# Kernel optimization log

Measured on AMD Instinct MI355X. Metric: run time of the kernel, lower is better.

The kernel has to match this reference:

```python
import jax, jax.numpy as jnp
import numpy as np

R = 1.1
SCALE = 100.0
BUMP_STEPS = 32
NUM_THETAS = 32
NUM_FEATURES = 128
N_NODES = 200000
NUM_GRAPHS = 128


def setup_inputs() -> dict:
    key = jax.random.key(0)
    k1, k2, k3 = jax.random.split(key, 3)
    x = jax.random.normal(k1, (N_NODES, NUM_FEATURES), dtype=jnp.float32)
    batch = jnp.sort(jax.random.randint(k2, (N_NODES,), 0, NUM_GRAPHS, dtype=jnp.int64))
    v = jax.random.uniform(k3, (NUM_THETAS, NUM_FEATURES), dtype=jnp.float32) - 0.5
    return {"x": x, "batch": batch, "num_graphs": NUM_GRAPHS, "v": v}


def reference(x, batch, num_graphs, v):
    # nh: node heights along each direction theta -> [N, T]
    nh = x @ v.T
    # linspace over filtration values -> [S]
    lin = jnp.linspace(-R, R, BUMP_STEPS, dtype=nh.dtype)
    # bump: sigmoid difference; second point is the constant pad value R
    # ecc: [N, S, T]  (node-major so segment_sum reduces the leading axis)
    ecc = (jax.nn.sigmoid(SCALE * (lin[None, :, None] - nh[:, None, :]))
           - jax.nn.sigmoid(SCALE * (lin - R))[None, :, None])
    # scatter-add per graph label -> [ng, S, T] == index_add over dim1 then movedim(0,1)
    ect = jax.ops.segment_sum(ecc, batch, num_segments=num_graphs)
    return ect
```

## Files before the change

kernel.cpp:

```cpp
#include <hip/hip_runtime.h>
#include <math.h>

#define NF 128
#define NT 32
#define NS 32
#define ATILE 64
#define ABLOCKS 3125
#define VSTRIDE 136
#define HPAD 33

typedef short bf16x8 __attribute__((ext_vector_type(8)));
typedef float floatx4 __attribute__((ext_vector_type(4)));

__device__ __forceinline__ float rcp_fast(float x) { return __builtin_amdgcn_rcpf(x); }

__device__ __forceinline__ void split_bf16(float f, unsigned short& h, unsigned short& l) {
    unsigned u  = __float_as_uint(f);
    unsigned r  = u + 0x7FFFu + ((u >> 16) & 1u);
    unsigned hb = r & 0xFFFF0000u;
    h = (unsigned short)(hb >> 16);
    float rem = f - __uint_as_float(hb);
    unsigned u2 = __float_as_uint(rem);
    unsigned r2 = u2 + 0x7FFFu + ((u2 >> 16) & 1u);
    l = (unsigned short)(r2 >> 16);
}

__device__ __forceinline__ void split8(float4 a, float4 b, bf16x8& h8, bf16x8& l8) {
    unsigned short h[8], l[8];
    split_bf16(a.x, h[0], l[0]); split_bf16(a.y, h[1], l[1]);
    split_bf16(a.z, h[2], l[2]); split_bf16(a.w, h[3], l[3]);
    split_bf16(b.x, h[4], l[4]); split_bf16(b.y, h[5], l[5]);
    split_bf16(b.z, h[6], l[6]); split_bf16(b.w, h[7], l[7]);
    h8 = (bf16x8){(short)h[0],(short)h[1],(short)h[2],(short)h[3],
                  (short)h[4],(short)h[5],(short)h[6],(short)h[7]};
    l8 = (bf16x8){(short)l[0],(short)l[1],(short)l[2],(short)l[3],
                  (short)l[4],(short)l[5],(short)l[6],(short)l[7]};
}

__global__ __launch_bounds__(256, 7)
void ect_fused(const float* __restrict__ x,
               const int* __restrict__ batch,
               const float* __restrict__ v,
               float* __restrict__ out)
{
    __shared__ __align__(16) unsigned short vh[NT * VSTRIDE];
    __shared__ __align__(16) unsigned short vl[NT * VSTRIDE];
    __shared__ int   batch_lds[ATILE];
    __shared__ float corr[NT * HPAD];
    __shared__ float cnt_lds;
    __shared__ int   qcnt[4];

    const int tid  = threadIdx.x;
    const int blk  = blockIdx.x;
    const int w    = tid >> 6;
    const int lane = tid & 63;
    const int mrow = lane & 15;
    const int quad = lane >> 4;

    #pragma unroll
    for (int j = 0; j < 4; ++j) {
        int idx4 = j * 256 + tid;
        int row  = idx4 >> 5;
        int f4   = idx4 & 31;
        float4 val = *(const float4*)&v[(size_t)row * NF + f4 * 4];
        unsigned short h0,h1,h2,h3,l0,l1,l2,l3;
        split_bf16(val.x, h0, l0); split_bf16(val.y, h1, l1);
        split_bf16(val.z, h2, l2); split_bf16(val.w, h3, l3);
        uint2 hh, ll;
        hh.x = (unsigned)h0 | ((unsigned)h1 << 16); hh.y = (unsigned)h2 | ((unsigned)h3 << 16);
        ll.x = (unsigned)l0 | ((unsigned)l1 << 16); ll.y = (unsigned)l2 | ((unsigned)l3 << 16);
        *(uint2*)&vh[row * VSTRIDE + f4 * 4] = hh;
        *(uint2*)&vl[row * VSTRIDE + f4 * 4] = ll;
    }
    if (tid < ATILE) batch_lds[tid] = batch[blk * ATILE + tid];

    const size_t arow = (size_t)blk * ATILE + w * 16 + mrow;
    const float* __restrict__ xrow = x + arow * NF + quad * 8;

    floatx4 acc0 = {0.f, 0.f, 0.f, 0.f};
    floatx4 acc1 = {0.f, 0.f, 0.f, 0.f};

    bf16x8 ah[4], al[4];
    #pragma unroll
    for (int slice = 0; slice < 4; ++slice) {
        float4 a0 = *(const float4*)&xrow[slice * 32];
        float4 a1 = *(const float4*)&xrow[slice * 32 + 4];
        split8(a0, a1, ah[slice], al[slice]);
    }
    __syncthreads();

    const int b0base = mrow * VSTRIDE + quad * 8;
    const int b1base = (16 + mrow) * VSTRIDE + quad * 8;
    #pragma unroll
    for (int slice = 0; slice < 4; ++slice) {
        bf16x8 bh0 = *(bf16x8*)&vh[b0base + slice * 32];
        bf16x8 bl0 = *(bf16x8*)&vl[b0base + slice * 32];
        bf16x8 bh1 = *(bf16x8*)&vh[b1base + slice * 32];
        bf16x8 bl1 = *(bf16x8*)&vl[b1base + slice * 32];
        acc0 = __builtin_amdgcn_mfma_f32_16x16x32_bf16(ah[slice], bh0, acc0, 0, 0, 0);
        acc0 = __builtin_amdgcn_mfma_f32_16x16x32_bf16(ah[slice], bl0, acc0, 0, 0, 0);
        acc0 = __builtin_amdgcn_mfma_f32_16x16x32_bf16(al[slice], bh0, acc0, 0, 0, 0);
        acc1 = __builtin_amdgcn_mfma_f32_16x16x32_bf16(ah[slice], bh1, acc1, 0, 0, 0);
        acc1 = __builtin_amdgcn_mfma_f32_16x16x32_bf16(ah[slice], bl1, acc1, 0, 0, 0);
        acc1 = __builtin_amdgcn_mfma_f32_16x16x32_bf16(al[slice], bh1, acc1, 0, 0, 0);
    }
    __syncthreads();

    float* qf = (float*)vh;

    const float inv_dlin = 14.090909090909092f;
    const float Lw       = 10.23848093f;
    const float dlin     = 2.2f / 31.0f;
    const float L        = 144.26950408889634f;
    const float C1       = 8.2777115e-04f;

    const int g_first = batch_lds[0];
    const int g_last  = batch_lds[ATILE - 1];

    const int ft = tid & 31;
    const int sb = tid >> 5;
    float csk[4];
    #pragma unroll
    for (int k = 0; k < 4; ++k) {
        int s = sb + 8 * k;
        float lin_s = -1.1f + (float)s * dlin;
        csk[k] = rcp_fast(1.0f + __builtin_amdgcn_exp2f(L * (1.1f - lin_s)));
    }

    const float cH0 = 31.5f + 64.0f * (float)mrow;
    const float cH1 = cH0 + 1024.0f;
    const float lo0 = cH0 - 16.95f, hi0 = cH0 + 16.95f;
    const float lo1 = cH1 - 16.95f, hi1 = cH1 + 16.95f;

    for (int gp = g_first; gp <= g_last; ++gp) {
        for (int i = tid; i < NT * HPAD; i += 256) corr[i] = 0.0f;
        if (tid < ATILE) {
            unsigned long long m2 = __ballot(batch_lds[tid] == gp);
            if (tid == 0) cnt_lds = (float)__popcll(m2);
        }
        int wbase = w * 512;
        int c0 = 0, c1 = 0;
        #pragma unroll
        for (int reg = 0; reg < 4; ++reg) {
            bool ok = (batch_lds[w * 16 + quad * 4 + reg] == gp);
            {
                float zt = fmaf(acc0[reg], inv_dlin, cH0);
                bool full = ok && (zt > lo0) && (zt < hi0);
                unsigned long long m = __ballot(full);
                int pos = __builtin_amdgcn_mbcnt_hi((unsigned)(m >> 32),
                          __builtin_amdgcn_mbcnt_lo((unsigned)m, 0));
                if (full) qf[wbase + pos] = zt;
                wbase += __popcll(m);
                c0 += (ok && (zt <= lo0)) ? 1 : 0;
            }
            {
                float zt = fmaf(acc1[reg], inv_dlin, cH1);
                bool full = ok && (zt > lo1) && (zt < hi1);
                unsigned long long m = __ballot(full);
                int pos = __builtin_amdgcn_mbcnt_hi((unsigned)(m >> 32),
                          __builtin_amdgcn_mbcnt_lo((unsigned)m, 0));
                if (full) qf[wbase + pos] = zt;
                wbase += __popcll(m);
                c1 += (ok && (zt <= lo1)) ? 1 : 0;
            }
        }
        if (lane == 0) qcnt[w] = wbase - w * 512;
        __syncthreads();

        if (c0) atomicAdd(&corr[mrow * HPAD], (float)c0);
        if (c1) atomicAdd(&corr[(16 + mrow) * HPAD], (float)c1);
        for (int seg = 0; seg < 4; ++seg) {
            const int ne = qcnt[seg];
            for (int i = tid; i < ne; i += 256) {
                float zt  = qf[seg * 512 + i];
                float tf  = floorf(zt * 0.015625f);
                float z   = fmaf(tf, -64.0f, zt) - 16.0f;
                int   b   = (int)tf * HPAD;
                float s0f = ceilf(z - 1.45f);
                int   s0  = (int)s0f;
                float e0  = __builtin_amdgcn_exp2f(Lw * (z - s0f));
                float e1  = e0 * C1;
                float e2  = e1 * C1;
                float f0  = rcp_fast(1.0f + e0);
                float f1  = rcp_fast(1.0f + e1);
                float f2  = rcp_fast(1.0f + e2);
                int sA = max(s0, 0);
                atomicAdd(&corr[b + sA], f0);
                int sB = max(s0 + 1, 0);
                if (sB < 32) atomicAdd(&corr[b + sB], f1 - f0);
                int sC = max(s0 + 2, 0);
                if (sC < 32) atomicAdd(&corr[b + sC], f2 - f1);
                int sD = s0 + 3;
                if (sD < 32) atomicAdd(&corr[b + sD], 1.0f - f2);
            }
        }
        __syncthreads();

        {
            const int grp = tid >> 5;
            const int sc  = tid & 31;
            for (int row = grp; row < NT; row += 8) {
                float val = corr[row * HPAD + sc];
                #pragma unroll
                for (int d = 1; d < 32; d <<= 1) {
                    float nbr = __shfl_up(val, d, 32);
                    if (sc >= d) val += nbr;
                }
                corr[row * HPAD + sc] = val;
            }
        }
        __syncthreads();

        #pragma unroll
        for (int k = 0; k < 4; ++k) {
            int s = sb + 8 * k;
            float val = corr[ft * HPAD + s] - cnt_lds * csk[k];
            atomicAdd(&out[(size_t)gp * (NS * NT) + s * NT + ft], val);
        }
        if (gp < g_last) __syncthreads();
    }
}

extern "C" void kernel_launch(void* const* d_in, const int* in_sizes, int n_in,
                              void* d_out, int out_size, void* d_ws, size_t ws_size,
                              hipStream_t stream) {
    const float* x     = (const float*)d_in[0];
    const int*   batch = (const int*)d_in[1];
    const float* v     = (const float*)d_in[3];
    float*       out   = (float*)d_out;

    hipMemsetAsync(d_out, 0, (size_t)out_size * sizeof(float), stream);
    ect_fused<<<dim3(ABLOCKS), dim3(256), 0, stream>>>(x, batch, v, out);
}
```

Before: 183.6 us.

## Double node tile per block and deposit bumps directly instead of compacting

Each block now handles 128 nodes in two MFMA passes, which halves the block count and the per-block fixed costs: splitting v into bf16 hi/lo, the per-graph corr reset and scan, and the global atomics to out. The ballot-based compaction queue in LDS and the separate loop that drained it are removed. Each lane now computes the sigmoid terms for its own in-window heights and adds them into corr with LDS atomics. The divergent per-lane deposits may leave SIMD lanes idle, and the occupancy hint drops from 7 to 5 blocks per CU, which lowers latency hiding.

```diff
diff --git a/kernel.cpp b/kernel.cpp
--- a/kernel.cpp
+++ b/kernel.cpp
@@ -1,11 +1,12 @@
 #include <hip/hip_runtime.h>
 #include <math.h>
 
+#define N_NODES 200000
 #define NF 128
 #define NT 32
 #define NS 32
-#define ATILE 64
-#define ABLOCKS 3125
+#define ATILE 128
+#define ABLOCKS 1563
 #define VSTRIDE 136
 #define HPAD 33
 
@@ -37,7 +38,22 @@
                   (short)l[4],(short)l[5],(short)l[6],(short)l[7]};
 }
 
-__global__ __launch_bounds__(256, 7)
+__device__ __forceinline__ void deposit(float* corr, int b, float z, float Lw, float C1) {
+    float s0f = ceilf(z - 1.45f);
+    int   s0  = (int)s0f;
+    float e0  = __builtin_amdgcn_exp2f(Lw * (z - s0f));
+    float e1  = e0 * C1;
+    float e2  = e1 * C1;
+    float f0  = rcp_fast(1.0f + e0);
+    float f1  = rcp_fast(1.0f + e1);
+    float f2  = rcp_fast(1.0f + e2);
+    atomicAdd(&corr[b + max(s0, 0)], f0);
+    int sB = max(s0 + 1, 0); if (sB < 32) atomicAdd(&corr[b + sB], f1 - f0);
+    int sC = max(s0 + 2, 0); if (sC < 32) atomicAdd(&corr[b + sC], f2 - f1);
+    int sD = s0 + 3;         if (sD < 32) atomicAdd(&corr[b + sD], 1.0f - f2);
+}
+
+__global__ __launch_bounds__(256, 5)
 void ect_fused(const float* __restrict__ x,
                const int* __restrict__ batch,
                const float* __restrict__ v,
@@ -47,8 +63,7 @@
     __shared__ __align__(16) unsigned short vl[NT * VSTRIDE];
     __shared__ int   batch_lds[ATILE];
     __shared__ float corr[NT * HPAD];
-    __shared__ float cnt_lds;
-    __shared__ int   qcnt[4];
+    __shared__ float cnt_part[2];
 
     const int tid  = threadIdx.x;
     const int blk  = blockIdx.x;
@@ -72,19 +87,27 @@
         *(uint2*)&vh[row * VSTRIDE + f4 * 4] = hh;
         *(uint2*)&vl[row * VSTRIDE + f4 * 4] = ll;
     }
-    if (tid < ATILE) batch_lds[tid] = batch[blk * ATILE + tid];
-
-    const size_t arow = (size_t)blk * ATILE + w * 16 + mrow;
-    const float* __restrict__ xrow = x + arow * NF + quad * 8;
-
-    floatx4 acc0 = {0.f, 0.f, 0.f, 0.f};
-    floatx4 acc1 = {0.f, 0.f, 0.f, 0.f};
+    const int base   = blk * ATILE;
+    const int nvalid = min(ATILE, N_NODES - base);
+    if (tid < ATILE) {
+        int gi = base + tid;
+        batch_lds[tid] = (gi < N_NODES) ? batch[gi] : -1;
+    }
+
+    const int r0  = w * 16 + mrow;
+    const int gi0 = min(base + r0,      N_NODES - 1);
+    const int gi1 = min(base + 64 + r0, N_NODES - 1);
+    const float* __restrict__ x0 = x + (size_t)gi0 * NF + quad * 8;
+    const float* __restrict__ x1 = x + (size_t)gi1 * NF + quad * 8;
+
+    floatx4 acc0[2] = {(floatx4){0.f,0.f,0.f,0.f}, (floatx4){0.f,0.f,0.f,0.f}};
+    floatx4 acc1[2] = {(floatx4){0.f,0.f,0.f,0.f}, (floatx4){0.f,0.f,0.f,0.f}};
 
     bf16x8 ah[4], al[4];
     #pragma unroll
     for (int slice = 0; slice < 4; ++slice) {
-        float4 a0 = *(const float4*)&xrow[slice * 32];
-        float4 a1 = *(const float4*)&xrow[slice * 32 + 4];
+        float4 a0 = *(const float4*)&x0[slice * 32];
+        float4 a1 = *(const float4*)&x0[slice * 32 + 4];
         split8(a0, a1, ah[slice], al[slice]);
     }
     __syncthreads();
@@ -97,16 +120,32 @@
         bf16x8 bl0 = *(bf16x8*)&vl[b0base + slice * 32];
         bf16x8 bh1 = *(bf16x8*)&vh[b1base + slice * 32];
         bf16x8 bl1 = *(bf16x8*)&vl[b1base + slice * 32];
-        acc0 = __builtin_amdgcn_mfma_f32_16x16x32_bf16(ah[slice], bh0, acc0, 0, 0, 0);
-        acc0 = __builtin_amdgcn_mfma_f32_16x16x32_bf16(ah[slice], bl0, acc0, 0, 0, 0);
-        acc0 = __builtin_amdgcn_mfma_f32_16x16x32_bf16(al[slice], bh0, acc0, 0, 0, 0);
-        acc1 = __builtin_amdgcn_mfma_f32_16x16x32_bf16(ah[slice], bh1, acc1, 0, 0, 0);
-        acc1 = __builtin_amdgcn_mfma_f32_16x16x32_bf16(ah[slice], bl1, acc1, 0, 0, 0);
-        acc1 = __builtin_amdgcn_mfma_f32_16x16x32_bf16(al[slice], bh1, acc1, 0, 0, 0);
-    }
-    __syncthreads();
-
-    float* qf = (float*)vh;
+        acc0[0] = __builtin_amdgcn_mfma_f32_16x16x32_bf16(ah[slice], bh0, acc0[0], 0, 0, 0);
+        acc0[0] = __builtin_amdgcn_mfma_f32_16x16x32_bf16(ah[slice], bl0, acc0[0], 0, 0, 0);
+        acc0[0] = __builtin_amdgcn_mfma_f32_16x16x32_bf16(al[slice], bh0, acc0[0], 0, 0, 0);
+        acc1[0] = __builtin_amdgcn_mfma_f32_16x16x32_bf16(ah[slice], bh1, acc1[0], 0, 0, 0);
+        acc1[0] = __builtin_amdgcn_mfma_f32_16x16x32_bf16(ah[slice], bl1, acc1[0], 0, 0, 0);
+        acc1[0] = __builtin_amdgcn_mfma_f32_16x16x32_bf16(al[slice], bh1, acc1[0], 0, 0, 0);
+    }
+    #pragma unroll
+    for (int slice = 0; slice < 4; ++slice) {
+        float4 a0 = *(const float4*)&x1[slice * 32];
+        float4 a1 = *(const float4*)&x1[slice * 32 + 4];
+        split8(a0, a1, ah[slice], al[slice]);
+    }
+    #pragma unroll
+    for (int slice = 0; slice < 4; ++slice) {
+        bf16x8 bh0 = *(bf16x8*)&vh[b0base + slice * 32];
+        bf16x8 bl0 = *(bf16x8*)&vl[b0base + slice * 32];
+        bf16x8 bh1 = *(bf16x8*)&vh[b1base + slice * 32];
+        bf16x8 bl1 = *(bf16x8*)&vl[b1base + slice * 32];
+        acc0[1] = __builtin_amdgcn_mfma_f32_16x16x32_bf16(ah[slice], bh0, acc0[1], 0, 0, 0);
+        acc0[1] = __builtin_amdgcn_mfma_f32_16x16x32_bf16(ah[slice], bl0, acc0[1], 0, 0, 0);
+        acc0[1] = __builtin_amdgcn_mfma_f32_16x16x32_bf16(al[slice], bh0, acc0[1], 0, 0, 0);
+        acc1[1] = __builtin_amdgcn_mfma_f32_16x16x32_bf16(ah[slice], bh1, acc1[1], 0, 0, 0);
+        acc1[1] = __builtin_amdgcn_mfma_f32_16x16x32_bf16(ah[slice], bl1, acc1[1], 0, 0, 0);
+        acc1[1] = __builtin_amdgcn_mfma_f32_16x16x32_bf16(al[slice], bh1, acc1[1], 0, 0, 0);
+    }
 
     const float inv_dlin = 14.090909090909092f;
     const float Lw       = 10.23848093f;
@@ -115,7 +154,7 @@
     const float C1       = 8.2777115e-04f;
 
     const int g_first = batch_lds[0];
-    const int g_last  = batch_lds[ATILE - 1];
+    const int g_last  = batch_lds[nvalid - 1];
 
     const int ft = tid & 31;
     const int sb = tid >> 5;
@@ -127,73 +166,40 @@
         csk[k] = rcp_fast(1.0f + __builtin_amdgcn_exp2f(L * (1.1f - lin_s)));
     }
 
-    const float cH0 = 31.5f + 64.0f * (float)mrow;
-    const float cH1 = cH0 + 1024.0f;
-    const float lo0 = cH0 - 16.95f, hi0 = cH0 + 16.95f;
-    const float lo1 = cH1 - 16.95f, hi1 = cH1 + 16.95f;
+    const int c0base = mrow * HPAD;
+    const int c1base = (16 + mrow) * HPAD;
 
     for (int gp = g_first; gp <= g_last; ++gp) {
         for (int i = tid; i < NT * HPAD; i += 256) corr[i] = 0.0f;
         if (tid < ATILE) {
-            unsigned long long m2 = __ballot(batch_lds[tid] == gp);
-            if (tid == 0) cnt_lds = (float)__popcll(m2);
-        }
-        int wbase = w * 512;
-        int c0 = 0, c1 = 0;
+            unsigned long long m = __ballot(batch_lds[tid] == gp);
+            if ((tid & 63) == 0) cnt_part[tid >> 6] = (float)__popcll(m);
+        }
+        __syncthreads();
+
+        float c0 = 0.f, c1 = 0.f;
         #pragma unroll
-        for (int reg = 0; reg < 4; ++reg) {
-            bool ok = (batch_lds[w * 16 + quad * 4 + reg] == gp);
-            {
-                float zt = fmaf(acc0[reg], inv_dlin, cH0);
-                bool full = ok && (zt > lo0) && (zt < hi0);
-                unsigned long long m = __ballot(full);
-                int pos = __builtin_amdgcn_mbcnt_hi((unsigned)(m >> 32),
-                          __builtin_amdgcn_mbcnt_lo((unsigned)m, 0));
-                if (full) qf[wbase + pos] = zt;
-                wbase += __popcll(m);
-                c0 += (ok && (zt <= lo0)) ? 1 : 0;
+        for (int mt = 0; mt < 2; ++mt) {
+            #pragma unroll
+            for (int reg = 0; reg < 4; ++reg) {
+                const int n = mt * 64 + w * 16 + quad * 4 + reg;
+                const bool ok = (batch_lds[n] == gp);
+                if (ok) {
+                    {
+                        float z = fmaf(acc0[mt][reg], inv_dlin, 15.5f);
+                        if (z <= -1.45f)      c0 += 1.0f;
+                        else if (z < 32.45f)  deposit(corr, c0base, z, Lw, C1);
+                    }
+                    {
+                        float z = fmaf(acc1[mt][reg], inv_dlin, 15.5f);
+                        if (z <= -1.45f)      c1 += 1.0f;
+                        else if (z < 32.45f)  deposit(corr, c1base, z, Lw, C1);
+                    }
+                }
             }
-            {
-                float zt = fmaf(acc1[reg], inv_dlin, cH1);
-                bool full = ok && (zt > lo1) && (zt < hi1);
-                unsigned long long m = __ballot(full);
-                int pos = __builtin_amdgcn_mbcnt_hi((unsigned)(m >> 32),
-                          __builtin_amdgcn_mbcnt_lo((unsigned)m, 0));
-                if (full) qf[wbase + pos] = zt;
-                wbase += __popcll(m);
-                c1 += (ok && (zt <= lo1)) ? 1 : 0;
-            }
-        }
-        if (lane == 0) qcnt[w] = wbase - w * 512;
-        __syncthreads();
-
-        if (c0) atomicAdd(&corr[mrow * HPAD], (float)c0);
-        if (c1) atomicAdd(&corr[(16 + mrow) * HPAD], (float)c1);
-        for (int seg = 0; seg < 4; ++seg) {
-            const int ne = qcnt[seg];
-            for (int i = tid; i < ne; i += 256) {
-                float zt  = qf[seg * 512 + i];
-                float tf  = floorf(zt * 0.015625f);
-                float z   = fmaf(tf, -64.0f, zt) - 16.0f;
-                int   b   = (int)tf * HPAD;
-                float s0f = ceilf(z - 1.45f);
-                int   s0  = (int)s0f;
-                float e0  = __builtin_amdgcn_exp2f(Lw * (z - s0f));
-                float e1  = e0 * C1;
-                float e2  = e1 * C1;
-                float f0  = rcp_fast(1.0f + e0);
-                float f1  = rcp_fast(1.0f + e1);
-                float f2  = rcp_fast(1.0f + e2);
-                int sA = max(s0, 0);
-                atomicAdd(&corr[b + sA], f0);
-                int sB = max(s0 + 1, 0);
-                if (sB < 32) atomicAdd(&corr[b + sB], f1 - f0);
-                int sC = max(s0 + 2, 0);
-                if (sC < 32) atomicAdd(&corr[b + sC], f2 - f1);
-                int sD = s0 + 3;
-                if (sD < 32) atomicAdd(&corr[b + sD], 1.0f - f2);
-            }
-        }
+        }
+        if (c0 != 0.f) atomicAdd(&corr[c0base], c0);
+        if (c1 != 0.f) atomicAdd(&corr[c1base], c1);
         __syncthreads();
 
         {
@@ -211,10 +217,11 @@
         }
         __syncthreads();
 
+        const float cnt = cnt_part[0] + cnt_part[1];
         #pragma unroll
         for (int k = 0; k < 4; ++k) {
             int s = sb + 8 * k;
-            float val = corr[ft * HPAD + s] - cnt_lds * csk[k];
+            float val = corr[ft * HPAD + s] - cnt * csk[k];
             atomicAdd(&out[(size_t)gp * (NS * NT) + s * NT + ft], val);
         }
         if (gp < g_last) __syncthreads();
```

New measurement: 226.7 us. 23.5% more time.
